# Performance work log

Measured on AMD Instinct MI355X. Metric: run time of the kernel, lower is better.

The kernel has to match this reference:

```python
import jax, jax.numpy as jnp
import numpy as np

N_NODES = 100000
N_EDGES = 3200000
IN_Z = 32
PROJ_H = 64
LOOP_D = 32
DEC_H = 64


def setup_inputs() -> dict:
    key = jax.random.key(0)
    ks = jax.random.split(key, 10)
    z_mod = jax.random.normal(ks[0], (N_NODES, IN_Z), dtype=jnp.float32)
    edge_index = jax.random.randint(ks[1], (2, N_EDGES), 0, N_NODES, dtype=jnp.int64)
    # loop_proj: Linear(32->64), ReLU, Linear(64->32)
    w1 = jax.random.normal(ks[2], (IN_Z, PROJ_H), dtype=jnp.float32) / np.sqrt(IN_Z)
    b1 = jnp.zeros((PROJ_H,), dtype=jnp.float32)
    w2 = jax.random.normal(ks[3], (PROJ_H, LOOP_D), dtype=jnp.float32) / np.sqrt(PROJ_H)
    b2 = jnp.zeros((LOOP_D,), dtype=jnp.float32)
    # decoder: Linear(2*loop_dim -> dec_hidden), ReLU, Linear(dec_hidden -> 1)
    dw1 = jax.random.normal(ks[4], (2 * LOOP_D, DEC_H), dtype=jnp.float32) / np.sqrt(2 * LOOP_D)
    db1 = jnp.zeros((DEC_H,), dtype=jnp.float32)
    dw2 = jax.random.normal(ks[5], (DEC_H, 1), dtype=jnp.float32) / np.sqrt(DEC_H)
    db2 = jnp.zeros((1,), dtype=jnp.float32)
    return {"z_mod": z_mod, "edge_index": edge_index, "w1": w1, "b1": b1,
            "w2": w2, "b2": b2, "dw1": dw1, "db1": db1, "dw2": dw2, "db2": db2}


def reference(z_mod, edge_index, w1, b1, w2, b2, dw1, db1, dw2, db2):
    # loop_proj: z_mod -> z_loop  [N, loop_dim]
    h = jax.nn.relu(z_mod @ w1 + b1)
    z_loop = h @ w2 + b2
    # edge-wise decoder: gather, concat, MLP
    zi = z_loop[edge_index[0]]            # [E, loop_dim]
    zj = z_loop[edge_index[1]]            # [E, loop_dim]
    he = jnp.concatenate([zi, zj], axis=-1)  # [E, 2*loop_dim]
    he = jax.nn.relu(he @ dw1 + db1)         # [E, dec_hidden]
    logits = (he @ dw2 + db2)[..., 0]        # [E]
    return logits
```

## Files before the change

kernel.cpp:

```cpp
#include <hip/hip_runtime.h>


typedef short bfrag4 __attribute__((ext_vector_type(4)));
typedef short s16x8  __attribute__((ext_vector_type(8)));
typedef float f32x4v __attribute__((ext_vector_type(4)));
typedef int   i32x4  __attribute__((ext_vector_type(4)));

#define N_NODES 100000
#define N_EDGES 3200000

__device__ __forceinline__ unsigned short f2bf(float f) {
    unsigned int i = __float_as_uint(f);
    unsigned int r = i + 0x7FFFu + ((i >> 16) & 1u);
    return (unsigned short)(r >> 16);
}

__device__ __forceinline__ float bf2f(unsigned short b) {
    unsigned int u = ((unsigned int)b) << 16;
    return __uint_as_float(u);
}

__device__ __forceinline__ bfrag4 cvt4(float x0, float x1, float x2, float x3) {
    bfrag4 v;
    v[0] = (short)f2bf(x0);
    v[1] = (short)f2bf(x1);
    v[2] = (short)f2bf(x2);
    v[3] = (short)f2bf(x3);
    return v;
}

__device__ __forceinline__ s16x8 dq8(long g, float s) {
    const int lo = (int)g;
    const int hi = (int)(g >> 32);
    s16x8 o;
#pragma unroll
    for (int j = 0; j < 4; ++j) {
        int bj = (lo << (24 - 8 * j)) >> 24;
        o[j] = (short)f2bf((float)bj * s);
    }
#pragma unroll
    for (int j = 0; j < 4; ++j) {
        int bj = (hi << (24 - 8 * j)) >> 24;
        o[4 + j] = (short)f2bf((float)bj * s);
    }
    return o;
}

__global__ __launch_bounds__(256) void node_proj_kernel(
    const float* __restrict__ z_mod,
    const float* __restrict__ w1,
    const float* __restrict__ b1,
    const float* __restrict__ w2,
    const float* __restrict__ b2,
    char*           __restrict__ z8,
    unsigned short* __restrict__ scg)
{
    __shared__ unsigned short hbuf[4][16 * 72];

    const int tid  = threadIdx.x;
    const int wave = tid >> 6;
    const int lane = tid & 63;
    const int quad = lane >> 4;
    const int col  = lane & 15;

    bfrag4 bw1[2][4];
    float  bias1[4];
    for (int t = 0; t < 4; ++t) {
        const int n = col + 16 * t;
        for (int s = 0; s < 2; ++s)
            for (int j = 0; j < 4; ++j)
                bw1[s][t][j] = (short)f2bf(w1[(s * 16 + quad * 4 + j) * 64 + n]);
        bias1[t] = b1[n];
    }
    bfrag4 bw2[4][2];
    float  bias2[2];
    for (int t = 0; t < 2; ++t) {
        const int n = col + 16 * t;
        for (int s = 0; s < 4; ++s)
            for (int j = 0; j < 4; ++j)
                bw2[s][t][j] = (short)f2bf(w2[(s * 16 + quad * 4 + j) * 32 + n]);
        bias2[t] = b2[n];
    }

    unsigned short* hrow = &hbuf[wave][0];

    const int gwave  = blockIdx.x * 4 + wave;
    const int nwaves = gridDim.x * 4;
    const int ntiles = N_NODES / 16;

    for (int tile = gwave; tile < ntiles; tile += nwaves) {
        const int node0 = tile * 16;
        const float* zrow = z_mod + (size_t)(node0 + col) * 32;

        f32x4v za0 = *(const f32x4v*)(zrow + 0 * 16 + quad * 4);
        f32x4v za1 = *(const f32x4v*)(zrow + 1 * 16 + quad * 4);
        bfrag4 a10 = cvt4(za0[0], za0[1], za0[2], za0[3]);
        bfrag4 a11 = cvt4(za1[0], za1[1], za1[2], za1[3]);

        f32x4v acc[4];
        for (int t = 0; t < 4; ++t) {
            f32x4v c = {bias1[t], bias1[t], bias1[t], bias1[t]};
            c = __builtin_amdgcn_mfma_f32_16x16x16bf16_1k(a10, bw1[0][t], c, 0, 0, 0);
            c = __builtin_amdgcn_mfma_f32_16x16x16bf16_1k(a11, bw1[1][t], c, 0, 0, 0);
            acc[t] = c;
        }

        for (int t = 0; t < 4; ++t)
            for (int r = 0; r < 4; ++r) {
                float v = acc[t][r];
                v = v > 0.f ? v : 0.f;
                hrow[(quad * 4 + r) * 72 + (col + 16 * t)] = f2bf(v);
            }
        asm volatile("" ::: "memory");

        f32x4v acc2[2];
        for (int t = 0; t < 2; ++t)
            acc2[t] = (f32x4v){bias2[t], bias2[t], bias2[t], bias2[t]};
        for (int s = 0; s < 4; ++s) {
            bfrag4 a2 = *(const bfrag4*)(hrow + col * 72 + s * 16 + quad * 4);
            for (int t = 0; t < 2; ++t)
                acc2[t] = __builtin_amdgcn_mfma_f32_16x16x16bf16_1k(a2, bw2[s][t], acc2[t], 0, 0, 0);
        }
        asm volatile("" ::: "memory");

        float am[4];
        for (int r = 0; r < 4; ++r)
            am[r] = fmaxf(fabsf(acc2[0][r]), fabsf(acc2[1][r]));
        for (int mask = 1; mask <= 8; mask <<= 1)
            for (int r = 0; r < 4; ++r)
                am[r] = fmaxf(am[r], __shfl_xor(am[r], mask, 64));
        const float gm = fmaxf(fmaxf(am[0], am[1]), fmaxf(am[2], am[3]));
        const float inv = 127.f / fmaxf(gm, 1e-30f);

        char* hb = (char*)hrow;
        for (int r = 0; r < 4; ++r)
            for (int t = 0; t < 2; ++t) {
                int q = (int)rintf(acc2[t][r] * inv);
                hb[(quad * 4 + r) * 32 + (col + 16 * t)] = (char)q;
            }
        if (col == 0)
            scg[(node0 >> 2) + quad] = f2bf(gm * (1.f / 127.f));
        asm volatile("" ::: "memory");

        *(unsigned long long*)(z8 + (size_t)node0 * 32 + lane * 8) =
            *(const unsigned long long*)(hb + lane * 8);
        asm volatile("" ::: "memory");
    }
}

__global__ __launch_bounds__(256) void edge_dec_kernel(
    const int*            __restrict__ eidx,
    const char*           __restrict__ z8,
    const unsigned short* __restrict__ scg,
    const float*          __restrict__ dw1,
    const float*          __restrict__ db1,
    const float*          __restrict__ dw2,
    const float*          __restrict__ db2,
    float* __restrict__ out)
{
    __shared__ i32x4 slds4[3128];
    unsigned short* slds = (unsigned short*)slds4;

    const int tid  = threadIdx.x;
    const int lane = tid & 63;
    const int quad = lane >> 4;
    const int col  = lane & 15;

    for (int i = tid; i < 3128; i += 256)
        slds4[i] = ((const i32x4*)scg)[i];

    s16x8 aw[2][4];
    f32x4v bias1v[4];
    float  w2v[4][4];
    for (int mt = 0; mt < 4; ++mt) {
        const int h = 16 * mt + col;
        for (int s = 0; s < 2; ++s)
            for (int j = 0; j < 8; ++j)
                aw[s][mt][j] = (short)f2bf(dw1[(32 * s + quad * 8 + j) * 64 + h]);
        for (int r = 0; r < 4; ++r) {
            bias1v[mt][r] = db1[16 * mt + quad * 4 + r];
            w2v[mt][r]    = dw2[16 * mt + quad * 4 + r];
        }
    }
    const float bias2 = db2[0];

    __syncthreads();

    const int gwave  = blockIdx.x * 4 + (tid >> 6);
    const int nwaves = gridDim.x * 4;
    const int npairs = N_EDGES / 32;

    const int qoff = quad * 8;

    int sA = eidx[gwave * 32 + col];
    int sB = eidx[gwave * 32 + 16 + col];
    int dA = eidx[N_EDGES + gwave * 32 + col];
    int dB = eidx[N_EDGES + gwave * 32 + 16 + col];

    for (int p = gwave; p < npairs; p += nwaves) {
        const int e0 = p * 32;

        long gA0 = *(const long*)(z8 + sA * 32 + qoff);
        long gA1 = *(const long*)(z8 + dA * 32 + qoff);
        long gB0 = *(const long*)(z8 + sB * 32 + qoff);
        long gB1 = *(const long*)(z8 + dB * 32 + qoff);

        float scA0 = bf2f(slds[sA >> 2]);
        float scA1 = bf2f(slds[dA >> 2]);
        float scB0 = bf2f(slds[sB >> 2]);
        float scB1 = bf2f(slds[dB >> 2]);

        const int pn = p + nwaves;
        const int pc = pn < npairs ? pn : gwave;
        sA = eidx[pc * 32 + col];
        sB = eidx[pc * 32 + 16 + col];
        dA = eidx[N_EDGES + pc * 32 + col];
        dB = eidx[N_EDGES + pc * 32 + 16 + col];

        s16x8 fA0 = dq8(gA0, scA0);
        s16x8 fA1 = dq8(gA1, scA1);
        s16x8 fB0 = dq8(gB0, scB0);
        s16x8 fB1 = dq8(gB1, scB1);

        f32x4v accA[4], accB[4];
        for (int mt = 0; mt < 4; ++mt) {
            f32x4v c = __builtin_amdgcn_mfma_f32_16x16x32_bf16(aw[0][mt], fA0, bias1v[mt], 0, 0, 0);
            accA[mt] = __builtin_amdgcn_mfma_f32_16x16x32_bf16(aw[1][mt], fA1, c, 0, 0, 0);
        }
        for (int mt = 0; mt < 4; ++mt) {
            f32x4v c = __builtin_amdgcn_mfma_f32_16x16x32_bf16(aw[0][mt], fB0, bias1v[mt], 0, 0, 0);
            accB[mt] = __builtin_amdgcn_mfma_f32_16x16x32_bf16(aw[1][mt], fB1, c, 0, 0, 0);
        }

        float pA = 0.f, pB = 0.f;
        for (int mt = 0; mt < 4; ++mt)
            for (int r = 0; r < 4; ++r) {
                float vA = accA[mt][r]; vA = vA > 0.f ? vA : 0.f;
                float vB = accB[mt][r]; vB = vB > 0.f ? vB : 0.f;
                pA += vA * w2v[mt][r];
                pB += vB * w2v[mt][r];
            }
        pA += __shfl_xor(pA, 16, 64);
        pA += __shfl_xor(pA, 32, 64);
        pB += __shfl_xor(pB, 16, 64);
        pB += __shfl_xor(pB, 32, 64);

        if (lane < 32) {
            float v = (lane < 16 ? pA : pB) + bias2;
            out[e0 + lane] = v;
        }
    }
}

extern "C" void kernel_launch(void* const* d_in, const int* in_sizes, int n_in,
                              void* d_out, int out_size, void* d_ws, size_t ws_size,
                              hipStream_t stream) {
    const float* z_mod = (const float*)d_in[0];
    const int*   eidx  = (const int*)d_in[1];
    const float* w1    = (const float*)d_in[2];
    const float* b1    = (const float*)d_in[3];
    const float* w2    = (const float*)d_in[4];
    const float* b2    = (const float*)d_in[5];
    const float* dw1   = (const float*)d_in[6];
    const float* db1   = (const float*)d_in[7];
    const float* dw2   = (const float*)d_in[8];
    const float* db2   = (const float*)d_in[9];
    float* out = (float*)d_out;

    char*           z8  = (char*)d_ws;
    unsigned short* scg = (unsigned short*)((char*)d_ws + (size_t)N_NODES * 32);

    node_proj_kernel<<<512, 256, 0, stream>>>(z_mod, w1, b1, w2, b2, z8, scg);
    edge_dec_kernel<<<768, 256, 0, stream>>>(eidx, z8, scg, dw1, db1, dw2, db2, out);
}
```

Before: 166.9 us.

## Use int8 MFMA for edge decoder with quantized weights, drop LDS scale table

The edge decoder now quantizes the first decoder weight matrix to int8 with a per-output-channel scale and runs i32 16x16x64 int8 MFMAs directly on the int8 node embeddings. This removes the per-element dequantize-to-bf16 step. Lanes are re-split so each lane loads 16 bytes of either the source or destination embedding, and masking splits the K dimension between the two endpoints. Per-node scales are now read from global memory instead of an LDS copy, and the grid grows from 768 to 2048 blocks. The cost is extra weight quantization error, and each tile now needs two MFMAs plus more float scaling work per accumulator.

Result: no change. 167.2 us (+0.2%).

```diff
diff --git a/kernel.cpp b/kernel.cpp
--- a/kernel.cpp
+++ b/kernel.cpp
@@ -2,7 +2,6 @@
 
 
 typedef short bfrag4 __attribute__((ext_vector_type(4)));
-typedef short s16x8  __attribute__((ext_vector_type(8)));
 typedef float f32x4v __attribute__((ext_vector_type(4)));
 typedef int   i32x4  __attribute__((ext_vector_type(4)));
 
@@ -27,23 +26,6 @@
     v[2] = (short)f2bf(x2);
     v[3] = (short)f2bf(x3);
     return v;
-}
-
-__device__ __forceinline__ s16x8 dq8(long g, float s) {
-    const int lo = (int)g;
-    const int hi = (int)(g >> 32);
-    s16x8 o;
-#pragma unroll
-    for (int j = 0; j < 4; ++j) {
-        int bj = (lo << (24 - 8 * j)) >> 24;
-        o[j] = (short)f2bf((float)bj * s);
-    }
-#pragma unroll
-    for (int j = 0; j < 4; ++j) {
-        int bj = (hi << (24 - 8 * j)) >> 24;
-        o[4 + j] = (short)f2bf((float)bj * s);
-    }
-    return o;
 }
 
 __global__ __launch_bounds__(256) void node_proj_kernel(
@@ -158,90 +140,110 @@
     const float*          __restrict__ db2,
     float* __restrict__ out)
 {
-    __shared__ i32x4 slds4[3128];
-    unsigned short* slds = (unsigned short*)slds4;
-
     const int tid  = threadIdx.x;
     const int lane = tid & 63;
     const int quad = lane >> 4;
     const int col  = lane & 15;
-
-    for (int i = tid; i < 3128; i += 256)
-        slds4[i] = ((const i32x4*)scg)[i];
-
-    s16x8 aw[2][4];
-    f32x4v bias1v[4];
-    float  w2v[4][4];
+    const int ss   = quad >> 1;
+    const int hf   = quad & 1;
+
+    i32x4  awq[4];
+    float  wscv[4];
     for (int mt = 0; mt < 4; ++mt) {
-        const int h = 16 * mt + col;
-        for (int s = 0; s < 2; ++s)
-            for (int j = 0; j < 8; ++j)
-                aw[s][mt][j] = (short)f2bf(dw1[(32 * s + quad * 8 + j) * 64 + h]);
+        const int m = 16 * mt + col;
+        float w[16];
+        float mx = 0.f;
+        for (int j = 0; j < 16; ++j) {
+            w[j] = dw1[(quad * 16 + j) * 64 + m];
+            mx = fmaxf(mx, fabsf(w[j]));
+        }
+        mx = fmaxf(mx, __shfl_xor(mx, 16, 64));
+        mx = fmaxf(mx, __shfl_xor(mx, 32, 64));
+        wscv[mt] = mx * (1.f / 127.f);
+        const float winv = 127.f / fmaxf(mx, 1e-30f);
+        i32x4 a;
+        for (int rr = 0; rr < 4; ++rr) {
+            int pk = 0;
+            for (int bi = 0; bi < 4; ++bi) {
+                int q = (int)rintf(w[rr * 4 + bi] * winv);
+                pk |= (q & 0xFF) << (8 * bi);
+            }
+            a[rr] = pk;
+        }
+        awq[mt] = a;
+    }
+    float wsce[4][4], bias1v[4][4], w2v[4][4];
+    for (int mt = 0; mt < 4; ++mt)
         for (int r = 0; r < 4; ++r) {
+            wsce[mt][r]   = __shfl(wscv[mt], quad * 4 + r, 64);
             bias1v[mt][r] = db1[16 * mt + quad * 4 + r];
             w2v[mt][r]    = dw2[16 * mt + quad * 4 + r];
         }
-    }
     const float bias2 = db2[0];
-
-    __syncthreads();
+    const int mlo = (quad < 2) ? -1 : 0;
+    const int mhi = ~mlo;
 
     const int gwave  = blockIdx.x * 4 + (tid >> 6);
     const int nwaves = gridDim.x * 4;
     const int npairs = N_EDGES / 32;
 
-    const int qoff = quad * 8;
-
-    int sA = eidx[gwave * 32 + col];
-    int sB = eidx[gwave * 32 + 16 + col];
-    int dA = eidx[N_EDGES + gwave * 32 + col];
-    int dB = eidx[N_EDGES + gwave * 32 + 16 + col];
+    const int iofs = ss * N_EDGES + col;
+
+    int iA = eidx[gwave * 32 + iofs];
+    int iB = eidx[gwave * 32 + 16 + iofs];
 
     for (int p = gwave; p < npairs; p += nwaves) {
         const int e0 = p * 32;
 
-        long gA0 = *(const long*)(z8 + sA * 32 + qoff);
-        long gA1 = *(const long*)(z8 + dA * 32 + qoff);
-        long gB0 = *(const long*)(z8 + sB * 32 + qoff);
-        long gB1 = *(const long*)(z8 + dB * 32 + qoff);
-
-        float scA0 = bf2f(slds[sA >> 2]);
-        float scA1 = bf2f(slds[dA >> 2]);
-        float scB0 = bf2f(slds[sB >> 2]);
-        float scB1 = bf2f(slds[dB >> 2]);
+        i32x4 gA = *(const i32x4*)(z8 + (size_t)iA * 32 + hf * 16);
+        i32x4 gB = *(const i32x4*)(z8 + (size_t)iB * 32 + hf * 16);
+        float scA = bf2f(scg[iA >> 2]);
+        float scB = bf2f(scg[iB >> 2]);
 
         const int pn = p + nwaves;
         const int pc = pn < npairs ? pn : gwave;
-        sA = eidx[pc * 32 + col];
-        sB = eidx[pc * 32 + 16 + col];
-        dA = eidx[N_EDGES + pc * 32 + col];
-        dB = eidx[N_EDGES + pc * 32 + 16 + col];
-
-        s16x8 fA0 = dq8(gA0, scA0);
-        s16x8 fA1 = dq8(gA1, scA1);
-        s16x8 fB0 = dq8(gB0, scB0);
-        s16x8 fB1 = dq8(gB1, scB1);
-
-        f32x4v accA[4], accB[4];
+        iA = eidx[pc * 32 + iofs];
+        iB = eidx[pc * 32 + 16 + iofs];
+
+        const i32x4 zc = {0, 0, 0, 0};
+
+        i32x4 b1, b2;
+        for (int i = 0; i < 4; ++i) { b1[i] = gA[i] & mlo; b2[i] = gA[i] & mhi; }
+        i32x4 a1[4], a2[4];
         for (int mt = 0; mt < 4; ++mt) {
-            f32x4v c = __builtin_amdgcn_mfma_f32_16x16x32_bf16(aw[0][mt], fA0, bias1v[mt], 0, 0, 0);
-            accA[mt] = __builtin_amdgcn_mfma_f32_16x16x32_bf16(aw[1][mt], fA1, c, 0, 0, 0);
-        }
-        for (int mt = 0; mt < 4; ++mt) {
-            f32x4v c = __builtin_amdgcn_mfma_f32_16x16x32_bf16(aw[0][mt], fB0, bias1v[mt], 0, 0, 0);
-            accB[mt] = __builtin_amdgcn_mfma_f32_16x16x32_bf16(aw[1][mt], fB1, c, 0, 0, 0);
-        }
-
-        float pA = 0.f, pB = 0.f;
+            a1[mt] = __builtin_amdgcn_mfma_i32_16x16x64_i8(awq[mt], b1, zc, 0, 0, 0);
+            a2[mt] = __builtin_amdgcn_mfma_i32_16x16x64_i8(awq[mt], b2, zc, 0, 0, 0);
+        }
+        float si = __shfl(scA, col, 64);
+        float sj = __shfl(scA, 32 + col, 64);
+        float pA = 0.f;
         for (int mt = 0; mt < 4; ++mt)
             for (int r = 0; r < 4; ++r) {
-                float vA = accA[mt][r]; vA = vA > 0.f ? vA : 0.f;
-                float vB = accB[mt][r]; vB = vB > 0.f ? vB : 0.f;
-                pA += vA * w2v[mt][r];
-                pB += vB * w2v[mt][r];
+                float t = (float)a1[mt][r] * si;
+                t = fmaf((float)a2[mt][r], sj, t);
+                float h = fmaf(t, wsce[mt][r], bias1v[mt][r]);
+                h = h > 0.f ? h : 0.f;
+                pA = fmaf(h, w2v[mt][r], pA);
             }
         pA += __shfl_xor(pA, 16, 64);
         pA += __shfl_xor(pA, 32, 64);
+
+        for (int i = 0; i < 4; ++i) { b1[i] = gB[i] & mlo; b2[i] = gB[i] & mhi; }
+        for (int mt = 0; mt < 4; ++mt) {
+            a1[mt] = __builtin_amdgcn_mfma_i32_16x16x64_i8(awq[mt], b1, zc, 0, 0, 0);
+            a2[mt] = __builtin_amdgcn_mfma_i32_16x16x64_i8(awq[mt], b2, zc, 0, 0, 0);
+        }
+        si = __shfl(scB, col, 64);
+        sj = __shfl(scB, 32 + col, 64);
+        float pB = 0.f;
+        for (int mt = 0; mt < 4; ++mt)
+            for (int r = 0; r < 4; ++r) {
+                float t = (float)a1[mt][r] * si;
+                t = fmaf((float)a2[mt][r], sj, t);
+                float h = fmaf(t, wsce[mt][r], bias1v[mt][r]);
+                h = h > 0.f ? h : 0.f;
+                pB = fmaf(h, w2v[mt][r], pB);
+            }
         pB += __shfl_xor(pB, 16, 64);
         pB += __shfl_xor(pB, 32, 64);
 
@@ -271,5 +273,5 @@
     unsigned short* scg = (unsigned short*)((char*)d_ws + (size_t)N_NODES * 32);
 
     node_proj_kernel<<<512, 256, 0, stream>>>(z_mod, w1, b1, w2, b2, z8, scg);
-    edge_dec_kernel<<<768, 256, 0, stream>>>(eidx, z8, scg, dw1, db1, dw2, db2, out);
-}
+    edge_dec_kernel<<<2048, 256, 0, stream>>>(eidx, z8, scg, dw1, db1, dw2, db2, out);
+}
```
